# Performance work log

Hardware: AMD Instinct MI355X
Metric: run time of the kernel (lower is better)

## Reference

```python
import jax, jax.numpy as jnp
import numpy as np

N_NODES = 50000
N_EDGES = 800000
D = 128  # in_dim == hidden_dim


def setup_inputs() -> dict:
    key = jax.random.key(0)
    k1, k2, k3, k4 = jax.random.split(key, 4)
    x = jax.random.normal(k1, (N_NODES, D), dtype=jnp.float32)
    edge_index = jax.random.randint(k2, (2, N_EDGES), 0, N_NODES, dtype=jnp.int64)
    # Glorot-ish scale for square weights
    scale = 1.0 / np.sqrt(D)
    W1 = jax.random.normal(k3, (D, D), dtype=jnp.float32) * scale
    W2 = jax.random.normal(k4, (D, D), dtype=jnp.float32) * scale
    b1 = jnp.zeros((D,), dtype=jnp.float32)
    b2 = jnp.zeros((D,), dtype=jnp.float32)
    return {"x": x, "edge_index": edge_index, "W1": W1, "b1": b1, "W2": W2, "b2": b2}


def _gcn_layer(x, W, b, src, dst, norm, n):
    # PyG GCNConv: h = x @ W, then symmetric-normalized scatter-add, then + bias
    h = x @ W                                   # [N, D] dense GEMM
    msg = h[src] * norm[:, None]                # [E', D] gather + scale
    out = jax.ops.segment_sum(msg, dst, num_segments=n)  # scatter-add
    return out + b


def reference(x, edge_index, W1, b1, W2, b2):
    n = x.shape[0]
    # add self-loops (GCNConv default add_self_loops=True)
    loops = jnp.arange(n, dtype=edge_index.dtype)
    src = jnp.concatenate([edge_index[0], loops])
    dst = jnp.concatenate([edge_index[1], loops])
    # symmetric normalization: deg^{-1/2}[src] * deg^{-1/2}[dst]
    deg = jax.ops.segment_sum(jnp.ones_like(src, dtype=x.dtype), dst, num_segments=n)
    dinv = jax.lax.rsqrt(jnp.maximum(deg, 1.0))  # deg >= 1 due to self-loops
    norm = dinv[src] * dinv[dst]
    # layer 1: conv -> relu (dropout is identity in eval mode)
    h = jax.nn.relu(_gcn_layer(x, W1, b1, src, dst, norm, n))
    # layer 2 (cut='c2'): conv -> relu
    h = jax.nn.relu(_gcn_layer(h, W2, b2, src, dst, norm, n))
    return h
```

## Files before the change

### kernel.cpp

```cpp
#include <hip/hip_runtime.h>
#include <hip/hip_fp16.h>

#define NN 50000
#define NE 800000
#define DD 128
#define NSTRIP 3125
#define NB 196
#define CHUNK 4096
#define MAXB 6144
#define ZROW NN

#define OF_LCNT  0
#define OF_LOFS  50176
#define OF_DINV  100352
#define OF_DEG   150352
#define OF_OFFS2 200352
#define OF_TMP2  300352
#define OF_CSRU  1103168
#define OF_H1    1705280
#define OF_H2    4905344
#define OF_W1H   8105408
#define OF_W1L   8113600
#define OF_W2H   8121792
#define OF_W2L   8129984

typedef __attribute__((ext_vector_type(8))) short bf8_t;
typedef __attribute__((ext_vector_type(8))) unsigned short us8;
typedef __attribute__((ext_vector_type(4))) float f32x4;

static __device__ __forceinline__ unsigned short f2bf(float f) {
    unsigned int u = __float_as_uint(f);
    unsigned int r = (u + 0x7fffu + ((u >> 16) & 1u)) >> 16;
    return (unsigned short)r;
}
static __device__ __forceinline__ float bf2f(unsigned short h) {
    return __uint_as_float(((unsigned int)h) << 16);
}
static __device__ __forceinline__ unsigned short f2h(float f) {
    return __half_as_ushort(__float2half(f));
}
static __device__ __forceinline__ float h2f(unsigned short u) {
    return __half2float(__ushort_as_half(u));
}

__global__ __launch_bounds__(256) void k_zero(int* __restrict__ deg,
                                              ushort* __restrict__ h1,
                                              ushort* __restrict__ h2) {
    int g = blockIdx.x * 256 + threadIdx.x;
    if (g < NN) deg[g] = 0;
    if (g < 64) ((unsigned int*)(h1 + (size_t)ZROW * DD))[g] = 0u;
    else if (g < 128) ((unsigned int*)(h2 + (size_t)ZROW * DD))[g - 64] = 0u;
}

__global__ __launch_bounds__(256) void k_ws(
        const float* __restrict__ W1, const float* __restrict__ W2,
        ushort* __restrict__ w1h, ushort* __restrict__ w1l,
        ushort* __restrict__ w2h, ushort* __restrict__ w2l,
        const int* __restrict__ src, const int* __restrict__ dst,
        int* __restrict__ lcnt_g, int* __restrict__ lofs_g,
        unsigned int* __restrict__ tmp2, int* __restrict__ deg) {
    __shared__ int lcnt[256];
    __shared__ int lsc[256];
    __shared__ int lcur[256];
    int tid = threadIdx.x;
    if (blockIdx.x < 16) {
        int gg = blockIdx.x * 256 + tid;
        const float* W = (gg < 2048) ? W1 : W2;
        ushort* wh = (gg < 2048) ? w1h : w2h;
        ushort* wl = (gg < 2048) ? w1l : w2l;
        int g = gg & 2047;
        int ntile = g >> 8;
        int kk = (g >> 6) & 3;
        int lane = g & 63;
        int k0 = kk * 32 + ((lane >> 4) * 8);
        int col = ntile * 16 + (lane & 15);
#pragma unroll
        for (int j = 0; j < 8; ++j) {
            float w = W[(k0 + j) * DD + col];
            unsigned short h = f2bf(w);
            wh[(size_t)g * 8 + j] = h;
            wl[(size_t)g * 8 + j] = f2bf(w - bf2f(h));
        }
        return;
    }
    int blk = blockIdx.x - 16;
    lcnt[tid] = 0;
    __syncthreads();
    int e0 = blk * CHUNK;
    int e1 = e0 + CHUNK; if (e1 > NE) e1 = NE;
    for (int e = e0 + tid; e < e1; e += 256) {
        int d = dst[e];
        atomicAdd(&lcnt[d >> 8], 1);
        atomicAdd(&deg[d], 1);
    }
    __syncthreads();
    int v = lcnt[tid];
    lsc[tid] = v;
    __syncthreads();
    for (int o = 1; o < 256; o <<= 1) {
        int t = (tid >= o) ? lsc[tid - o] : 0;
        __syncthreads();
        lsc[tid] += t;
        __syncthreads();
    }
    int excl = lsc[tid] - v;
    lcnt_g[tid * 196 + blk] = v;
    lofs_g[tid * 196 + blk] = excl;
    lcur[tid] = excl;
    __syncthreads();
    for (int e = e0 + tid; e < e1; e += 256) {
        int d = dst[e], s = src[e];
        int b = d >> 8;
        int r = atomicAdd(&lcur[b], 1);
        tmp2[blk * CHUNK + r] = ((unsigned int)s << 8) | (unsigned int)(d & 255);
    }
}

__global__ __launch_bounds__(256) void k_sg(
        const int* __restrict__ lcnt_g, const int* __restrict__ lofs_g,
        const unsigned int* __restrict__ tmp2, const int* __restrict__ deg,
        ushort* __restrict__ csru, int2* __restrict__ offs2,
        float* __restrict__ dinv,
        const float* __restrict__ X,
        const ushort* __restrict__ wh, const ushort* __restrict__ wl,
        ushort* __restrict__ H1) {
    __shared__ unsigned int ent[MAXB];
    __shared__ int c[256];
    __shared__ int p[256];
    __shared__ int o[256];
    __shared__ int cnt[256];
    __shared__ int boff[256];
    __shared__ int cur[256];
    int tid = threadIdx.x;
    if (blockIdx.x < 196) {
        int b = blockIdx.x;
        int cv = (tid < 196) ? lcnt_g[b * 196 + tid] : 0;
        o[tid] = (tid < 196) ? lofs_g[b * 196 + tid] : 0;
        c[tid] = cv;
        p[tid] = cv;
        cnt[tid] = 0;
        __syncthreads();
        for (int s = 1; s < 256; s <<= 1) {
            int t = (tid >= s) ? p[tid - s] : 0;
            __syncthreads();
            p[tid] += t;
            __syncthreads();
        }
        int nb = p[255];
        for (int i = tid; i < nb; i += 256) {
            int lo = 0, hi = 255;
#pragma unroll
            for (int it = 0; it < 8; ++it) {
                int mid = (lo + hi) >> 1;
                if (p[mid] > i) hi = mid; else lo = mid + 1;
            }
            int blk = lo;
            int j = i - (p[blk] - c[blk]);
            unsigned int e = tmp2[blk * CHUNK + o[blk] + j];
            ent[i] = e;
            atomicAdd(&cnt[e & 255], 1);
        }
        __syncthreads();
        int v = cnt[tid];
        boff[tid] = v;
        __syncthreads();
        for (int s = 1; s < 256; s <<= 1) {
            int t = (tid >= s) ? boff[tid - s] : 0;
            __syncthreads();
            boff[tid] += t;
            __syncthreads();
        }
        int excl = boff[tid] - v;
        int base = b * MAXB;
        int node = b * 256 + tid;
        if (node < NN) {
            offs2[node] = make_int2(base + excl, base + excl + v);
            dinv[node] = rsqrtf((float)(v + 1));
        }
        cur[tid] = excl;
        __syncthreads();
        for (int i = tid; i < nb; i += 256) {
            unsigned int e = ent[i];
            int bin = e & 255;
            int r = atomicAdd(&cur[bin], 1);
            csru[base + r] = (ushort)(e >> 8);
        }
        return;
    }
    int wave = tid >> 6;
    int lane = tid & 63;
    int strip = (blockIdx.x - 196) * 4 + wave;
    if (strip >= NSTRIP) return;
    int rb = strip << 4;
    int m = lane & 15;
    int quad = lane >> 4;
    const float* ar = X + (size_t)(rb + m) * DD;
    f32x4 acc[8];
#pragma unroll
    for (int t = 0; t < 8; ++t) acc[t] = (f32x4){0.f, 0.f, 0.f, 0.f};
#pragma unroll
    for (int kk = 0; kk < 4; ++kk) {
        float4 xa = *(const float4*)(ar + kk * 32 + quad * 8);
        float4 xb = *(const float4*)(ar + kk * 32 + quad * 8 + 4);
        float xs[8] = {xa.x, xa.y, xa.z, xa.w, xb.x, xb.y, xb.z, xb.w};
        bf8_t ah, al;
#pragma unroll
        for (int j = 0; j < 8; ++j) {
            unsigned short hh = f2bf(xs[j]);
            ah[j] = (short)hh;
            al[j] = (short)f2bf(xs[j] - bf2f(hh));
        }
#pragma unroll
        for (int t = 0; t < 8; ++t) {
            size_t bo = ((size_t)(t * 4 + kk) * 64 + lane) * 8;
            bf8_t bh = *(const bf8_t*)(wh + bo);
            bf8_t bl = *(const bf8_t*)(wl + bo);
            acc[t] = __builtin_amdgcn_mfma_f32_16x16x32_bf16(ah, bh, acc[t], 0, 0, 0);
            acc[t] = __builtin_amdgcn_mfma_f32_16x16x32_bf16(ah, bl, acc[t], 0, 0, 0);
            acc[t] = __builtin_amdgcn_mfma_f32_16x16x32_bf16(al, bh, acc[t], 0, 0, 0);
        }
    }
    int4 dg = *(const int4*)(deg + rb + quad * 4);
    float dvv[4] = {rsqrtf((float)(dg.x + 1)), rsqrtf((float)(dg.y + 1)),
                    rsqrtf((float)(dg.z + 1)), rsqrtf((float)(dg.w + 1))};
#pragma unroll
    for (int t = 0; t < 8; ++t) {
#pragma unroll
        for (int r = 0; r < 4; ++r)
            H1[(size_t)(rb + quad * 4 + r) * DD + t * 16 + m] =
                f2h(dvv[r] * acc[t][r]);
    }
}

__global__ __launch_bounds__(512) void k_aggmm(const ushort* __restrict__ h1,
                                               const float* __restrict__ dinv,
                                               const int2* __restrict__ offs2,
                                               const ushort* __restrict__ csru,
                                               const float* __restrict__ b1,
                                               const ushort* __restrict__ w2h,
                                               const ushort* __restrict__ w2l,
                                               ushort* __restrict__ h2) {
    __shared__ float xs[16][136];
    int wave = threadIdx.x >> 6;
    int lane = threadIdx.x & 63;
    int rb = blockIdx.x * 16;
    int q = lane >> 4;
    int l = lane & 15;
    const float* bp = b1 + 8 * l;
    for (int nn = 0; nn < 2; ++nn) {
        int node = rb + wave * 2 + nn;
        int2 oe = offs2[node];
        int e1 = oe.y;
        float a[8] = {0.f, 0.f, 0.f, 0.f, 0.f, 0.f, 0.f, 0.f};
        for (int eb = oe.x; eb < e1; eb += 32) {
            int s[8];
#pragma unroll
            for (int j = 0; j < 8; ++j) {
                int e = eb + q + 4 * j;
                int er = (e < e1) ? e : (e1 - 1);
                er = (er < 0) ? 0 : er;
                int sv = (int)csru[er];
                s[j] = (e < e1) ? sv : ZROW;
            }
            us8 v[8];
#pragma unroll
            for (int j = 0; j < 8; ++j)
                v[j] = *(const us8*)(h1 + ((size_t)s[j] << 7) + 8 * l);
#pragma unroll
            for (int j = 0; j < 8; ++j) {
#pragma unroll
                for (int d = 0; d < 8; ++d) a[d] += h2f(v[j][d]);
            }
        }
        if (q == 0) {
            us8 v = *(const us8*)(h1 + ((size_t)node << 7) + 8 * l);
#pragma unroll
            for (int j = 0; j < 8; ++j) a[j] += h2f(v[j]);
        }
#pragma unroll
        for (int j = 0; j < 8; ++j) {
            a[j] += __shfl_xor(a[j], 16, 64);
            a[j] += __shfl_xor(a[j], 32, 64);
        }
        if (q == 0) {
            float dnode = dinv[node];
            float* xr = &xs[wave * 2 + nn][8 * l];
#pragma unroll
            for (int j = 0; j < 8; ++j)
                xr[j] = fmaxf(dnode * a[j] + bp[j], 0.f);
        }
    }
    __syncthreads();
    int m = lane & 15;
    int quad = lane >> 4;
    int t = wave;
    f32x4 acc = (f32x4){0.f, 0.f, 0.f, 0.f};
#pragma unroll
    for (int kk = 0; kk < 4; ++kk) {
        const float* xr = &xs[m][kk * 32 + quad * 8];
        float4 xa = *(const float4*)xr;
        float4 xb = *(const float4*)(xr + 4);
        float xv[8] = {xa.x, xa.y, xa.z, xa.w, xb.x, xb.y, xb.z, xb.w};
        bf8_t ah, al;
#pragma unroll
        for (int j = 0; j < 8; ++j) {
            unsigned short hh = f2bf(xv[j]);
            ah[j] = (short)hh;
            al[j] = (short)f2bf(xv[j] - bf2f(hh));
        }
        size_t bo = ((size_t)(t * 4 + kk) * 64 + lane) * 8;
        bf8_t bh = *(const bf8_t*)(w2h + bo);
        bf8_t bl = *(const bf8_t*)(w2l + bo);
        acc = __builtin_amdgcn_mfma_f32_16x16x32_bf16(ah, bh, acc, 0, 0, 0);
        acc = __builtin_amdgcn_mfma_f32_16x16x32_bf16(ah, bl, acc, 0, 0, 0);
        acc = __builtin_amdgcn_mfma_f32_16x16x32_bf16(al, bh, acc, 0, 0, 0);
    }
    float4 dv4 = *(const float4*)(dinv + rb + quad * 4);
    float dvv[4] = {dv4.x, dv4.y, dv4.z, dv4.w};
#pragma unroll
    for (int r = 0; r < 4; ++r)
        h2[(size_t)(rb + quad * 4 + r) * DD + t * 16 + m] = f2h(dvv[r] * acc[r]);
}

__global__ __launch_bounds__(256) void k_agg(const ushort* __restrict__ h,
                                             const float* __restrict__ dinv,
                                             const int2* __restrict__ offs2,
                                             const ushort* __restrict__ csru,
                                             const float* __restrict__ bias,
                                             float* __restrict__ outf) {
    int wave = threadIdx.x >> 6;
    int lane = threadIdx.x & 63;
    int node = blockIdx.x * 4 + wave;
    int q = lane >> 4;
    int l = lane & 15;
    int2 oe = offs2[node];
    int e1 = oe.y;
    float a[8] = {0.f, 0.f, 0.f, 0.f, 0.f, 0.f, 0.f, 0.f};
    for (int eb = oe.x; eb < e1; eb += 32) {
        int s[8];
#pragma unroll
        for (int j = 0; j < 8; ++j) {
            int e = eb + q + 4 * j;
            int er = (e < e1) ? e : (e1 - 1);
            er = (er < 0) ? 0 : er;
            int sv = (int)csru[er];
            s[j] = (e < e1) ? sv : ZROW;
        }
        us8 v[8];
#pragma unroll
        for (int j = 0; j < 8; ++j)
            v[j] = *(const us8*)(h + ((size_t)s[j] << 7) + 8 * l);
#pragma unroll
        for (int j = 0; j < 8; ++j) {
#pragma unroll
            for (int d = 0; d < 8; ++d) a[d] += h2f(v[j][d]);
        }
    }
    if (q == 0) {
        us8 v = *(const us8*)(h + ((size_t)node << 7) + 8 * l);
#pragma unroll
        for (int j = 0; j < 8; ++j) a[j] += h2f(v[j]);
    }
#pragma unroll
    for (int j = 0; j < 8; ++j) {
        a[j] += __shfl_xor(a[j], 16, 64);
        a[j] += __shfl_xor(a[j], 32, 64);
    }
    if (q == 0) {
        float dnode = dinv[node];
        float* op = outf + (size_t)node * DD + 8 * l;
        const float* bp = bias + 8 * l;
        float4 o0, o1;
        o0.x = fmaxf(dnode * a[0] + bp[0], 0.f);
        o0.y = fmaxf(dnode * a[1] + bp[1], 0.f);
        o0.z = fmaxf(dnode * a[2] + bp[2], 0.f);
        o0.w = fmaxf(dnode * a[3] + bp[3], 0.f);
        o1.x = fmaxf(dnode * a[4] + bp[4], 0.f);
        o1.y = fmaxf(dnode * a[5] + bp[5], 0.f);
        o1.z = fmaxf(dnode * a[6] + bp[6], 0.f);
        o1.w = fmaxf(dnode * a[7] + bp[7], 0.f);
        *(float4*)op = o0;
        *(float4*)(op + 4) = o1;
    }
}

extern "C" void kernel_launch(void* const* d_in, const int* in_sizes, int n_in,
                              void* d_out, int out_size, void* d_ws, size_t ws_size,
                              hipStream_t stream) {
    const float* x  = (const float*)d_in[0];
    const int*   ei = (const int*)d_in[1];
    const float* W1 = (const float*)d_in[2];
    const float* b1 = (const float*)d_in[3];
    const float* W2 = (const float*)d_in[4];
    const float* b2 = (const float*)d_in[5];
    float* out = (float*)d_out;

    const int* src = ei;
    const int* dst = ei + NE;

    int*          wsi  = (int*)d_ws;
    float*        wsf  = (float*)d_ws;
    ushort*       wsu  = (ushort*)d_ws;
    unsigned int* wsuw = (unsigned int*)d_ws;
    int*    lcnt_g = wsi + OF_LCNT;
    int*    lofs_g = wsi + OF_LOFS;
    float*  dinv   = wsf + OF_DINV;
    int*    deg    = wsi + OF_DEG;
    int2*   offs2  = (int2*)(wsi + OF_OFFS2);
    unsigned int* tmp2 = wsuw + OF_TMP2;
    ushort* csru   = wsu + (size_t)OF_CSRU * 2;
    ushort* h1     = wsu + (size_t)OF_H1 * 2;
    ushort* h2     = wsu + (size_t)OF_H2 * 2;
    ushort* w1h    = wsu + (size_t)OF_W1H * 2;
    ushort* w1l    = wsu + (size_t)OF_W1L * 2;
    ushort* w2h    = wsu + (size_t)OF_W2H * 2;
    ushort* w2l    = wsu + (size_t)OF_W2L * 2;

    hipLaunchKernelGGL(k_zero, dim3(196), dim3(256), 0, stream, deg, h1, h2);
    hipLaunchKernelGGL(k_ws, dim3(16 + 196), dim3(256), 0, stream,
                       W1, W2, w1h, w1l, w2h, w2l,
                       src, dst, lcnt_g, lofs_g, tmp2, deg);
    hipLaunchKernelGGL(k_sg, dim3(196 + (NSTRIP + 3) / 4), dim3(256), 0, stream,
                       lcnt_g, lofs_g, tmp2, deg, csru, offs2, dinv,
                       x, w1h, w1l, h1);
    hipLaunchKernelGGL(k_aggmm, dim3(NSTRIP), dim3(512), 0, stream,
                       h1, dinv, offs2, csru, b1, w2h, w2l, h2);
    hipLaunchKernelGGL(k_agg, dim3(NN / 4), dim3(256), 0, stream,
                       h2, dinv, offs2, csru, b2, out);
}
```

Before: 217.3 us.

## Build CSR via global degree histogram, scan, and atomic scatter

Replaces the two-pass bucketed counting sort (per-chunk local histograms, transposed offset tables, shared-memory regrouping) with a simpler CSR build: a global atomic degree histogram, a per-bucket scan that pads each row to a multiple of four with zero-row entries, and a scatter kernel using per-node global atomic cursors. The aggregation loops now skip the per-slot clamping and select, predicating gathers on the remaining count instead. This drops the tmp2 staging buffer and one shared-memory-heavy pass, but adds an extra kernel launch and global atomics on 50k counters. Edge order within a row becomes nondeterministic, so floating-point summation order varies between runs.

```diff
diff --git a/kernel.cpp b/kernel.cpp
--- a/kernel.cpp
+++ b/kernel.cpp
@@ -5,24 +5,22 @@
 #define NE 800000
 #define DD 128
 #define NSTRIP 3125
-#define NB 196
-#define CHUNK 4096
+#define NBUCK 196
 #define MAXB 6144
 #define ZROW NN
-
-#define OF_LCNT  0
-#define OF_LOFS  50176
-#define OF_DINV  100352
-#define OF_DEG   150352
-#define OF_OFFS2 200352
-#define OF_TMP2  300352
-#define OF_CSRU  1103168
-#define OF_H1    1705280
-#define OF_H2    4905344
-#define OF_W1H   8105408
-#define OF_W1L   8113600
-#define OF_W2H   8121792
-#define OF_W2L   8129984
+#define NHIST 208
+
+#define OF_DINV  0
+#define OF_DEG   50000
+#define OF_CUR   100000
+#define OF_OFFS2 150000
+#define OF_CSRU  250000
+#define OF_H1    852112
+#define OF_H2    4052176
+#define OF_W1H   7252240
+#define OF_W1L   7260432
+#define OF_W2H   7268624
+#define OF_W2L   7276816
 
 typedef __attribute__((ext_vector_type(8))) short bf8_t;
 typedef __attribute__((ext_vector_type(8))) unsigned short us8;
@@ -52,16 +50,11 @@
     else if (g < 128) ((unsigned int*)(h2 + (size_t)ZROW * DD))[g - 64] = 0u;
 }
 
-__global__ __launch_bounds__(256) void k_ws(
+__global__ __launch_bounds__(256) void k_hw(
         const float* __restrict__ W1, const float* __restrict__ W2,
         ushort* __restrict__ w1h, ushort* __restrict__ w1l,
         ushort* __restrict__ w2h, ushort* __restrict__ w2l,
-        const int* __restrict__ src, const int* __restrict__ dst,
-        int* __restrict__ lcnt_g, int* __restrict__ lofs_g,
-        unsigned int* __restrict__ tmp2, int* __restrict__ deg) {
-    __shared__ int lcnt[256];
-    __shared__ int lsc[256];
-    __shared__ int lcur[256];
+        const int* __restrict__ dst, int* __restrict__ deg) {
     int tid = threadIdx.x;
     if (blockIdx.x < 16) {
         int gg = blockIdx.x * 256 + tid;
@@ -83,107 +76,52 @@
         }
         return;
     }
-    int blk = blockIdx.x - 16;
-    lcnt[tid] = 0;
+    int g = (blockIdx.x - 16) * 256 + tid;
+    for (int e = g; e < NE; e += NHIST * 256)
+        atomicAdd(&deg[dst[e]], 1);
+}
+
+__global__ __launch_bounds__(256) void k_scan(const int* __restrict__ deg,
+                                              int2* __restrict__ offs2,
+                                              float* __restrict__ dinv,
+                                              int* __restrict__ cur,
+                                              ushort* __restrict__ csru) {
+    __shared__ int sc[256];
+    int b = blockIdx.x, tid = threadIdx.x;
+    int node = b * 256 + tid;
+    int dv = (node < NN) ? deg[node] : 0;
+    int p = (dv + 3) & ~3;
+    sc[tid] = p;
     __syncthreads();
-    int e0 = blk * CHUNK;
-    int e1 = e0 + CHUNK; if (e1 > NE) e1 = NE;
-    for (int e = e0 + tid; e < e1; e += 256) {
-        int d = dst[e];
-        atomicAdd(&lcnt[d >> 8], 1);
-        atomicAdd(&deg[d], 1);
-    }
-    __syncthreads();
-    int v = lcnt[tid];
-    lsc[tid] = v;
-    __syncthreads();
-    for (int o = 1; o < 256; o <<= 1) {
-        int t = (tid >= o) ? lsc[tid - o] : 0;
+    for (int s = 1; s < 256; s <<= 1) {
+        int t = (tid >= s) ? sc[tid - s] : 0;
         __syncthreads();
-        lsc[tid] += t;
+        sc[tid] += t;
         __syncthreads();
     }
-    int excl = lsc[tid] - v;
-    lcnt_g[tid * 196 + blk] = v;
-    lofs_g[tid * 196 + blk] = excl;
-    lcur[tid] = excl;
-    __syncthreads();
-    for (int e = e0 + tid; e < e1; e += 256) {
-        int d = dst[e], s = src[e];
-        int b = d >> 8;
-        int r = atomicAdd(&lcur[b], 1);
-        tmp2[blk * CHUNK + r] = ((unsigned int)s << 8) | (unsigned int)(d & 255);
-    }
-}
-
-__global__ __launch_bounds__(256) void k_sg(
-        const int* __restrict__ lcnt_g, const int* __restrict__ lofs_g,
-        const unsigned int* __restrict__ tmp2, const int* __restrict__ deg,
-        ushort* __restrict__ csru, int2* __restrict__ offs2,
-        float* __restrict__ dinv,
+    int start = b * MAXB + sc[tid] - p;
+    if (node < NN) {
+        offs2[node] = make_int2(start, start + p);
+        dinv[node] = rsqrtf((float)(dv + 1));
+        cur[node] = start;
+        for (int k = dv; k < p; ++k) csru[start + k] = (ushort)ZROW;
+    }
+}
+
+__global__ __launch_bounds__(256) void k_scg(
+        const int* __restrict__ src, const int* __restrict__ dst,
+        int* __restrict__ cur, ushort* __restrict__ csru,
+        const int* __restrict__ deg,
         const float* __restrict__ X,
         const ushort* __restrict__ wh, const ushort* __restrict__ wl,
         ushort* __restrict__ H1) {
-    __shared__ unsigned int ent[MAXB];
-    __shared__ int c[256];
-    __shared__ int p[256];
-    __shared__ int o[256];
-    __shared__ int cnt[256];
-    __shared__ int boff[256];
-    __shared__ int cur[256];
     int tid = threadIdx.x;
     if (blockIdx.x < 196) {
-        int b = blockIdx.x;
-        int cv = (tid < 196) ? lcnt_g[b * 196 + tid] : 0;
-        o[tid] = (tid < 196) ? lofs_g[b * 196 + tid] : 0;
-        c[tid] = cv;
-        p[tid] = cv;
-        cnt[tid] = 0;
-        __syncthreads();
-        for (int s = 1; s < 256; s <<= 1) {
-            int t = (tid >= s) ? p[tid - s] : 0;
-            __syncthreads();
-            p[tid] += t;
-            __syncthreads();
-        }
-        int nb = p[255];
-        for (int i = tid; i < nb; i += 256) {
-            int lo = 0, hi = 255;
-#pragma unroll
-            for (int it = 0; it < 8; ++it) {
-                int mid = (lo + hi) >> 1;
-                if (p[mid] > i) hi = mid; else lo = mid + 1;
-            }
-            int blk = lo;
-            int j = i - (p[blk] - c[blk]);
-            unsigned int e = tmp2[blk * CHUNK + o[blk] + j];
-            ent[i] = e;
-            atomicAdd(&cnt[e & 255], 1);
-        }
-        __syncthreads();
-        int v = cnt[tid];
-        boff[tid] = v;
-        __syncthreads();
-        for (int s = 1; s < 256; s <<= 1) {
-            int t = (tid >= s) ? boff[tid - s] : 0;
-            __syncthreads();
-            boff[tid] += t;
-            __syncthreads();
-        }
-        int excl = boff[tid] - v;
-        int base = b * MAXB;
-        int node = b * 256 + tid;
-        if (node < NN) {
-            offs2[node] = make_int2(base + excl, base + excl + v);
-            dinv[node] = rsqrtf((float)(v + 1));
-        }
-        cur[tid] = excl;
-        __syncthreads();
-        for (int i = tid; i < nb; i += 256) {
-            unsigned int e = ent[i];
-            int bin = e & 255;
-            int r = atomicAdd(&cur[bin], 1);
-            csru[base + r] = (ushort)(e >> 8);
+        int g = blockIdx.x * 256 + tid;
+        for (int e = g; e < NE; e += 196 * 256) {
+            int d = dst[e];
+            int r = atomicAdd(&cur[d], 1);
+            csru[r] = (ushort)src[e];
         }
         return;
     }
@@ -253,23 +191,21 @@
         int e1 = oe.y;
         float a[8] = {0.f, 0.f, 0.f, 0.f, 0.f, 0.f, 0.f, 0.f};
         for (int eb = oe.x; eb < e1; eb += 32) {
-            int s[8];
+            int rem = e1 - eb;
+            us8 v[8];
 #pragma unroll
             for (int j = 0; j < 8; ++j) {
-                int e = eb + q + 4 * j;
-                int er = (e < e1) ? e : (e1 - 1);
-                er = (er < 0) ? 0 : er;
-                int sv = (int)csru[er];
-                s[j] = (e < e1) ? sv : ZROW;
+                if (4 * j < rem) {
+                    int s = (int)csru[eb + 4 * j + q];
+                    v[j] = *(const us8*)(h1 + ((size_t)s << 7) + 8 * l);
+                }
             }
-            us8 v[8];
-#pragma unroll
-            for (int j = 0; j < 8; ++j)
-                v[j] = *(const us8*)(h1 + ((size_t)s[j] << 7) + 8 * l);
 #pragma unroll
             for (int j = 0; j < 8; ++j) {
-#pragma unroll
-                for (int d = 0; d < 8; ++d) a[d] += h2f(v[j][d]);
+                if (4 * j < rem) {
+#pragma unroll
+                    for (int d = 0; d < 8; ++d) a[d] += h2f(v[j][d]);
+                }
             }
         }
         if (q == 0) {
@@ -337,23 +273,21 @@
     int e1 = oe.y;
     float a[8] = {0.f, 0.f, 0.f, 0.f, 0.f, 0.f, 0.f, 0.f};
     for (int eb = oe.x; eb < e1; eb += 32) {
-        int s[8];
-#pragma unroll
-        for (int j = 0; j < 8; ++j) {
-            int e = eb + q + 4 * j;
-            int er = (e < e1) ? e : (e1 - 1);
-            er = (er < 0) ? 0 : er;
-            int sv = (int)csru[er];
-            s[j] = (e < e1) ? sv : ZROW;
-        }
+        int rem = e1 - eb;
         us8 v[8];
 #pragma unroll
-        for (int j = 0; j < 8; ++j)
-            v[j] = *(const us8*)(h + ((size_t)s[j] << 7) + 8 * l);
-#pragma unroll
-        for (int j = 0; j < 8; ++j) {
-#pragma unroll
-            for (int d = 0; d < 8; ++d) a[d] += h2f(v[j][d]);
+        for (int j = 0; j < 8; ++j) {
+            if (4 * j < rem) {
+                int s = (int)csru[eb + 4 * j + q];
+                v[j] = *(const us8*)(h + ((size_t)s << 7) + 8 * l);
+            }
+        }
+#pragma unroll
+        for (int j = 0; j < 8; ++j) {
+            if (4 * j < rem) {
+#pragma unroll
+                for (int d = 0; d < 8; ++d) a[d] += h2f(v[j][d]);
+            }
         }
     }
     if (q == 0) {
@@ -398,31 +332,28 @@
     const int* src = ei;
     const int* dst = ei + NE;
 
-    int*          wsi  = (int*)d_ws;
-    float*        wsf  = (float*)d_ws;
-    ushort*       wsu  = (ushort*)d_ws;
-    unsigned int* wsuw = (unsigned int*)d_ws;
-    int*    lcnt_g = wsi + OF_LCNT;
-    int*    lofs_g = wsi + OF_LOFS;
-    float*  dinv   = wsf + OF_DINV;
-    int*    deg    = wsi + OF_DEG;
-    int2*   offs2  = (int2*)(wsi + OF_OFFS2);
-    unsigned int* tmp2 = wsuw + OF_TMP2;
-    ushort* csru   = wsu + (size_t)OF_CSRU * 2;
-    ushort* h1     = wsu + (size_t)OF_H1 * 2;
-    ushort* h2     = wsu + (size_t)OF_H2 * 2;
-    ushort* w1h    = wsu + (size_t)OF_W1H * 2;
-    ushort* w1l    = wsu + (size_t)OF_W1L * 2;
-    ushort* w2h    = wsu + (size_t)OF_W2H * 2;
-    ushort* w2l    = wsu + (size_t)OF_W2L * 2;
+    int*    wsi  = (int*)d_ws;
+    float*  wsf  = (float*)d_ws;
+    ushort* wsu  = (ushort*)d_ws;
+    float*  dinv  = wsf + OF_DINV;
+    int*    deg   = wsi + OF_DEG;
+    int*    cur   = wsi + OF_CUR;
+    int2*   offs2 = (int2*)(wsi + OF_OFFS2);
+    ushort* csru  = wsu + (size_t)OF_CSRU * 2;
+    ushort* h1    = wsu + (size_t)OF_H1 * 2;
+    ushort* h2    = wsu + (size_t)OF_H2 * 2;
+    ushort* w1h   = wsu + (size_t)OF_W1H * 2;
+    ushort* w1l   = wsu + (size_t)OF_W1L * 2;
+    ushort* w2h   = wsu + (size_t)OF_W2H * 2;
+    ushort* w2l   = wsu + (size_t)OF_W2L * 2;
 
     hipLaunchKernelGGL(k_zero, dim3(196), dim3(256), 0, stream, deg, h1, h2);
-    hipLaunchKernelGGL(k_ws, dim3(16 + 196), dim3(256), 0, stream,
-                       W1, W2, w1h, w1l, w2h, w2l,
-                       src, dst, lcnt_g, lofs_g, tmp2, deg);
-    hipLaunchKernelGGL(k_sg, dim3(196 + (NSTRIP + 3) / 4), dim3(256), 0, stream,
-                       lcnt_g, lofs_g, tmp2, deg, csru, offs2, dinv,
-                       x, w1h, w1l, h1);
+    hipLaunchKernelGGL(k_hw, dim3(16 + NHIST), dim3(256), 0, stream,
+                       W1, W2, w1h, w1l, w2h, w2l, dst, deg);
+    hipLaunchKernelGGL(k_scan, dim3(NBUCK), dim3(256), 0, stream,
+                       deg, offs2, dinv, cur, csru);
+    hipLaunchKernelGGL(k_scg, dim3(196 + (NSTRIP + 3) / 4), dim3(256), 0, stream,
+                       src, dst, cur, csru, deg, x, w1h, w1l, h1);
     hipLaunchKernelGGL(k_aggmm, dim3(NSTRIP), dim3(512), 0, stream,
                        h1, dinv, offs2, csru, b1, w2h, w2l, h2);
     hipLaunchKernelGGL(k_agg, dim3(NN / 4), dim3(256), 0, stream,
```

Result: slower. 265.3 us (+22.1%).
